# Optimization experiments

Measured on AMD Instinct MI355X. Metric: run time of the kernel, lower is better.

Reference implementation:

```python
import jax, jax.numpy as jnp
import numpy as np

N, E, B = 10000, 20000, 400
ND, ED, D = 32, 16, 64


def setup_inputs() -> dict:
    key = jax.random.key(0)
    ks = jax.random.split(key, 32)

    def lin(k, out_d, in_d):
        kw, kb = jax.random.split(k)
        s = 1.0 / np.sqrt(in_d)
        return (jax.random.uniform(kw, (out_d, in_d), jnp.float32, -s, s),
                jax.random.uniform(kb, (out_d,), jnp.float32, -s, s))

    W_in, b_in = lin(ks[0], D, ND)
    W_e1, b_e1 = lin(ks[1], D, ED)
    W_e2, b_e2 = lin(ks[2], D * D, D)
    b_conv = jax.random.uniform(ks[3], (D,), jnp.float32, -1/8.0, 1/8.0)
    W_ih, b_ih = lin(ks[4], 3 * D, D)
    W_hh, b_hh = lin(ks[5], 3 * D, D)
    W_ih_l, b_ih_l = lin(ks[6], 4 * D, 2 * D)
    W_hh_l, b_hh_l = lin(ks[7], 4 * D, D)
    W_o1, b_o1 = lin(ks[8], D, 2 * D)
    W_o2, b_o2 = lin(ks[9], 1, D)

    x = jax.random.normal(ks[10], (N, ND), jnp.float32)
    edge_attr = jax.random.normal(ks[11], (E, ED), jnp.float32)
    edge_index = jax.random.randint(ks[12], (2, E), 0, N, jnp.int64)
    batch = jnp.sort(jax.random.randint(ks[13], (N,), 0, B, jnp.int64))

    return dict(x=x, edge_attr=edge_attr,
                W_in=W_in, b_in=b_in, W_e1=W_e1, b_e1=b_e1, W_e2=W_e2, b_e2=b_e2,
                b_conv=b_conv, W_ih=W_ih, b_ih=b_ih, W_hh=W_hh, b_hh=b_hh,
                W_ih_l=W_ih_l, b_ih_l=b_ih_l, W_hh_l=W_hh_l, b_hh_l=b_hh_l,
                W_o1=W_o1, b_o1=b_o1, W_o2=W_o2, b_o2=b_o2,
                edge_index=edge_index, batch=batch)


def reference(x, edge_attr, W_in, b_in, W_e1, b_e1, W_e2, b_e2, b_conv,
              W_ih, b_ih, W_hh, b_hh, W_ih_l, b_ih_l, W_hh_l, b_hh_l,
              W_o1, b_o1, W_o2, b_o2, edge_index, batch):
    src, dst = edge_index[0], edge_index[1]

    # in_linear
    out = jax.nn.relu(x @ W_in.T + b_in)            # [N, D]
    h = out                                          # GRU hidden (layer=1, seq=1)

    # edge-conditioned weights: MLP(edge_attr) -> [E, D, D]
    ew = (jax.nn.relu(edge_attr @ W_e1.T + b_e1) @ W_e2.T + b_e2).reshape(E, D, D)
    cnt = jnp.maximum(jax.ops.segment_sum(jnp.ones((E,), x.dtype), dst, N), 1.0)

    for _ in range(3):
        # NNConv: gather src nodes, per-edge matmul, scatter-mean to dst, + bias
        msg = jnp.einsum('ed,edf->ef', out[src], ew)                 # [E, D]
        agg = jax.ops.segment_sum(msg, dst, N) / cnt[:, None] + b_conv
        m = jax.nn.relu(agg)
        # GRU cell (torch gate order r, z, n)
        gi = m @ W_ih.T + b_ih
        gh = h @ W_hh.T + b_hh
        i_r, i_z, i_n = jnp.split(gi, 3, axis=-1)
        h_r, h_z, h_n = jnp.split(gh, 3, axis=-1)
        r = jax.nn.sigmoid(i_r + h_r)
        z = jax.nn.sigmoid(i_z + h_z)
        n = jnp.tanh(i_n + r * h_n)
        h = (1.0 - z) * n + z * h
        out = h

    # Set2Set pooling, processing_steps=3
    q_star = jnp.zeros((B, 2 * D), x.dtype)
    hl = jnp.zeros((B, D), x.dtype)
    cl = jnp.zeros((B, D), x.dtype)
    for _ in range(3):
        g = q_star @ W_ih_l.T + b_ih_l + hl @ W_hh_l.T + b_hh_l
        gi_, gf_, gg_, go_ = jnp.split(g, 4, axis=-1)   # torch order i,f,g,o
        cl = jax.nn.sigmoid(gf_) * cl + jax.nn.sigmoid(gi_) * jnp.tanh(gg_)
        hl = jax.nn.sigmoid(go_) * jnp.tanh(cl)
        q = hl                                           # [B, D]
        e = jnp.sum(out * q[batch], axis=-1)             # [N]
        mmax = jax.ops.segment_max(e, batch, B)
        a = jnp.exp(e - mmax[batch])
        a = a / jax.ops.segment_sum(a, batch, B)[batch]
        r_ = jax.ops.segment_sum(a[:, None] * out, batch, B)  # [B, D]
        q_star = jnp.concatenate([q, r_], axis=-1)

    o = jax.nn.relu(q_star @ W_o1.T + b_o1) @ W_o2.T + b_o2
    return o.reshape(-1)
```

## Files before the change

### kernel.cpp

```cpp
#include <hip/hip_runtime.h>
#include <math.h>


#define Nn 10000
#define Ee 20000
#define Bb 400
#define KSTEPS 130
#define S2S_CHUNK 1024

typedef __attribute__((ext_vector_type(8))) short bf16x8_t;
typedef __attribute__((ext_vector_type(4))) float f32x4_t;

__device__ __forceinline__ float sigmoidf_(float x) { return 1.f / (1.f + expf(-x)); }

__device__ __forceinline__ void split8(const float* p, bf16x8_t& Ahi_, bf16x8_t& Alo_) {
    union { bf16x8_t v; unsigned u[4]; } hi, lo;
#pragma unroll
    for (int ii = 0; ii < 4; ++ii) {
        float pa = p[2 * ii], pb = p[2 * ii + 1];
        unsigned ua = __float_as_uint(pa), ub = __float_as_uint(pb);
        hi.u[ii] = (ua >> 16) | (ub & 0xFFFF0000u);
        float la = pa - __uint_as_float(ua & 0xFFFF0000u);
        float lb = pb - __uint_as_float(ub & 0xFFFF0000u);
        lo.u[ii] = (__float_as_uint(la) >> 16) | (__float_as_uint(lb) & 0xFFFF0000u);
    }
    Ahi_ = hi.v; Alo_ = lo.v;
}

__global__ __launch_bounds__(256) void k_in_linear(const float* __restrict__ x,
                                                   const float* __restrict__ Win,
                                                   const float* __restrict__ bin,
                                                   float* __restrict__ out) {
    int idx = blockIdx.x * 256 + threadIdx.x;
    if (idx >= Nn * 64) return;
    int n = idx >> 6, j = idx & 63;
    const float* xr = x + n * 32;
    const float* w = Win + j * 32;
    float acc = bin[j];
#pragma unroll
    for (int k = 0; k < 32; ++k) acc += xr[k] * w[k];
    out[idx] = fmaxf(acc, 0.f);
}

__global__ __launch_bounds__(256) void k_edge_mlp1(const float* __restrict__ ea,
                                                   const float* __restrict__ W1,
                                                   const float* __restrict__ b1,
                                                   float* __restrict__ eh) {
    int idx = blockIdx.x * 256 + threadIdx.x;
    if (idx >= Ee * 64) return;
    int e = idx >> 6, j = idx & 63;
    const float* ar = ea + e * 16;
    const float* w = W1 + j * 16;
    float acc = b1[j];
#pragma unroll
    for (int k = 0; k < 16; ++k) acc += ar[k] * w[k];
    eh[idx] = fmaxf(acc, 0.f);
}

__global__ __launch_bounds__(256) void k_make_Bfat(const float* __restrict__ W2,
                                                   const float* __restrict__ b2,
                                                   unsigned short* __restrict__ Bfat) {
    int idx = blockIdx.x * 256 + threadIdx.x;
    if (idx >= KSTEPS * 4096) return;
    int i  = idx & 7;
    int l  = (idx >> 3) & 63;
    int nq = (idx >> 9) & 3;
    int h  = (idx >> 11) & 1;
    int ks = idx >> 12;
    int kap = ks * 32 + (l >> 4) * 8 + i;
    int f = nq * 16 + (l & 15);
    float w;
    if (kap < 4096) {
        int q = kap >> 6, d = kap & 63;
        w = W2[(size_t)(d * 64 + f) * 64 + q];
    } else {
        int d = kap - 4096;
        w = b2[d * 64 + f];
    }
    unsigned u = __float_as_uint(w);
    unsigned short outv;
    if (h == 0) {
        outv = (unsigned short)(u >> 16);
    } else {
        float lo = w - __uint_as_float(u & 0xFFFF0000u);
        outv = (unsigned short)(__float_as_uint(lo) >> 16);
    }
    Bfat[idx] = outv;
}

__global__ __launch_bounds__(256) void k_make_Wg(const float* __restrict__ Wih,
                                                 const float* __restrict__ Whh,
                                                 unsigned short* __restrict__ Wg) {
    int idx = blockIdx.x * 256 + threadIdx.x;
    if (idx >= 4 * 2 * 16 * 64 * 8) return;
    int i  = idx & 7;
    int l  = (idx >> 3) & 63;
    int t  = (idx >> 9) & 15;
    int h  = (idx >> 13) & 1;
    int ks = idx >> 14;
    int k = ks * 32 + (l >> 4) * 8 + i;
    int u = t * 16 + (l & 15);
    int j = u & 63, part = u >> 6;
    float w = 0.f;
    if (part == 0) w = (k < 64) ? Wih[(size_t)j * 64 + k]          : Whh[(size_t)j * 64 + (k - 64)];
    if (part == 1) w = (k < 64) ? Wih[(size_t)(64 + j) * 64 + k]   : Whh[(size_t)(64 + j) * 64 + (k - 64)];
    if (part == 2) w = (k < 64) ? Wih[(size_t)(128 + j) * 64 + k]  : 0.f;
    if (part == 3) w = (k < 64) ? 0.f : Whh[(size_t)(128 + j) * 64 + (k - 64)];
    unsigned uu = __float_as_uint(w);
    unsigned short outv;
    if (h == 0) {
        outv = (unsigned short)(uu >> 16);
    } else {
        float lo = w - __uint_as_float(uu & 0xFFFF0000u);
        outv = (unsigned short)(__float_as_uint(lo) >> 16);
    }
    Wg[idx] = outv;
}

__global__ __launch_bounds__(256) void k_msg_mfma(const float* __restrict__ out,
                                                  const float* __restrict__ eh,
                                                  const unsigned short* __restrict__ Bfat,
                                                  const int* __restrict__ ei,
                                                  float* __restrict__ agg) {
    __shared__ float outs[64][68];
    __shared__ float ehs[64][68];
    __shared__ int dsts[64];
    int tid = threadIdx.x;
    int ebase = blockIdx.x * 64;
    int ksplit = blockIdx.y;

    {
        int el = tid >> 2, seg = tid & 3;
        int eg = ebase + el;
        bool v = eg < Ee;
        int s = 0, dn = 0;
        if (v) { s = ei[eg]; dn = ei[Ee + eg]; }
        if (seg == 0) dsts[el] = dn;
        const float* orow = out + (size_t)s * 64 + seg * 16;
        const float* erow = eh + (size_t)eg * 64 + seg * 16;
        float4 z = make_float4(0.f, 0.f, 0.f, 0.f);
#pragma unroll
        for (int c = 0; c < 4; ++c) {
            float4 ov = v ? *(const float4*)(orow + c * 4) : z;
            float4 ev = v ? *(const float4*)(erow + c * 4) : z;
            *(float4*)&outs[el][seg * 16 + c * 4] = ov;
            *(float4*)&ehs[el][seg * 16 + c * 4] = ev;
        }
    }
    __syncthreads();

    int lane = tid & 63;
    int wtile = tid >> 6;
    int m16 = lane & 15;
    int g = lane >> 4;
    int er = wtile * 16 + m16;

    f32x4_t acc[4];
#pragma unroll
    for (int nq = 0; nq < 4; ++nq) acc[nq] = (f32x4_t){0.f, 0.f, 0.f, 0.f};

    int ks0 = ksplit * 32 + (ksplit < 2 ? ksplit : 2);
    int ks1 = ks0 + (ksplit < 2 ? 33 : 32);

#pragma unroll 2
    for (int ks = ks0; ks < ks1; ++ks) {
        float ehq; int dbase;
        if (ks < 128) { ehq = ehs[er][ks >> 1]; dbase = (ks & 1) * 32 + g * 8; }
        else          { ehq = 1.f;              dbase = (ks - 128) * 32 + g * 8; }
        float4 o1 = *(const float4*)&outs[er][dbase];
        float4 o2 = *(const float4*)&outs[er][dbase + 4];
        float p[8] = {o1.x * ehq, o1.y * ehq, o1.z * ehq, o1.w * ehq,
                      o2.x * ehq, o2.y * ehq, o2.z * ehq, o2.w * ehq};
        bf16x8_t Ahi, Alo;
        split8(p, Ahi, Alo);
        const unsigned short* bstep = Bfat + (size_t)ks * 4096;
#pragma unroll
        for (int nq = 0; nq < 4; ++nq) {
            bf16x8_t bhi = *(const bf16x8_t*)(bstep + ((size_t)nq * 64 + lane) * 8);
            bf16x8_t blo = *(const bf16x8_t*)(bstep + ((size_t)(4 + nq) * 64 + lane) * 8);
            acc[nq] = __builtin_amdgcn_mfma_f32_16x16x32_bf16(Ahi, bhi, acc[nq], 0, 0, 0);
            acc[nq] = __builtin_amdgcn_mfma_f32_16x16x32_bf16(Ahi, blo, acc[nq], 0, 0, 0);
            acc[nq] = __builtin_amdgcn_mfma_f32_16x16x32_bf16(Alo, bhi, acc[nq], 0, 0, 0);
        }
    }

#pragma unroll
    for (int nq = 0; nq < 4; ++nq) {
#pragma unroll
        for (int r = 0; r < 4; ++r) {
            int el = wtile * 16 + g * 4 + r;
            int eg = ebase + el;
            if (eg < Ee)
                atomicAdd(&agg[(size_t)dsts[el] * 64 + nq * 16 + m16], acc[nq][r]);
        }
    }
}

__global__ __launch_bounds__(256) void k_gru_mfma(const float* __restrict__ agg,
                                                  const float* __restrict__ cnt,
                                                  const float* __restrict__ bconv,
                                                  const unsigned short* __restrict__ Wg,
                                                  const float* __restrict__ bih,
                                                  const float* __restrict__ bhh,
                                                  float* __restrict__ out) {
    __shared__ float ms[64][68];
    __shared__ float hs[64][68];
    int tid = threadIdx.x;
    int nbase = blockIdx.x * 64;

    {
        int nl = tid >> 2, seg = tid & 3;
        int ng = nbase + nl;
        bool v = ng < Nn;
        float c = v ? cnt[ng] : 1.f;
        c = c < 1.f ? 1.f : c;
        float rc = 1.f / c;
        const float* arow = agg + (size_t)ng * 64 + seg * 16;
        const float* hrow = out + (size_t)ng * 64 + seg * 16;
#pragma unroll
        for (int c4 = 0; c4 < 4; ++c4) {
            int col = seg * 16 + c4 * 4;
            float4 z = make_float4(0.f, 0.f, 0.f, 0.f);
            float4 av = v ? *(const float4*)(arow + c4 * 4) : z;
            float4 hv = v ? *(const float4*)(hrow + c4 * 4) : z;
            ms[nl][col + 0] = fmaxf(av.x * rc + bconv[col + 0], 0.f);
            ms[nl][col + 1] = fmaxf(av.y * rc + bconv[col + 1], 0.f);
            ms[nl][col + 2] = fmaxf(av.z * rc + bconv[col + 2], 0.f);
            ms[nl][col + 3] = fmaxf(av.w * rc + bconv[col + 3], 0.f);
            *(float4*)&hs[nl][col] = hv;
        }
    }
    __syncthreads();

    int lane = tid & 63;
    int wtile = tid >> 6;
    int m16 = lane & 15;
    int g = lane >> 4;
    int er = wtile * 16 + m16;

    f32x4_t acc[16];
#pragma unroll
    for (int t = 0; t < 16; ++t) acc[t] = (f32x4_t){0.f, 0.f, 0.f, 0.f};

#pragma unroll
    for (int ks = 0; ks < 4; ++ks) {
        const float* src = (ks < 2) ? &ms[er][ks * 32 + g * 8]
                                    : &hs[er][(ks - 2) * 32 + g * 8];
        float p[8];
#pragma unroll
        for (int ii = 0; ii < 8; ++ii) p[ii] = src[ii];
        bf16x8_t Ahi, Alo;
        split8(p, Ahi, Alo);
        const unsigned short* bstep = Wg + (size_t)ks * (2 * 16 * 512);
#pragma unroll
        for (int t = 0; t < 16; ++t) {
            bf16x8_t bhi = *(const bf16x8_t*)(bstep + ((size_t)t * 64 + lane) * 8);
            bf16x8_t blo = *(const bf16x8_t*)(bstep + ((size_t)(16 + t) * 64 + lane) * 8);
            acc[t] = __builtin_amdgcn_mfma_f32_16x16x32_bf16(Ahi, bhi, acc[t], 0, 0, 0);
            acc[t] = __builtin_amdgcn_mfma_f32_16x16x32_bf16(Ahi, blo, acc[t], 0, 0, 0);
            acc[t] = __builtin_amdgcn_mfma_f32_16x16x32_bf16(Alo, bhi, acc[t], 0, 0, 0);
        }
    }

#pragma unroll
    for (int t2 = 0; t2 < 4; ++t2) {
        int jj = t2 * 16 + m16;
        float br = bih[jj] + bhh[jj];
        float bz = bih[64 + jj] + bhh[64 + jj];
        float bin_ = bih[128 + jj];
        float bhn = bhh[128 + jj];
#pragma unroll
        for (int r = 0; r < 4; ++r) {
            int nl2 = wtile * 16 + g * 4 + r;
            int ng2 = nbase + nl2;
            if (ng2 >= Nn) continue;
            float rg = sigmoidf_(acc[t2][r] + br);
            float z  = sigmoidf_(acc[4 + t2][r] + bz);
            float nn = tanhf(acc[8 + t2][r] + bin_ + rg * (acc[12 + t2][r] + bhn));
            float hv = hs[nl2][jj];
            out[(size_t)ng2 * 64 + jj] = (1.f - z) * nn + z * hv;
        }
    }
}

__global__ __launch_bounds__(256) void k_count_deg(const int* __restrict__ ei,
                                                   float* __restrict__ cnt) {
    int e = blockIdx.x * 256 + threadIdx.x;
    if (e >= Ee) return;
    atomicAdd(&cnt[ei[Ee + e]], 1.f);
}

__global__ __launch_bounds__(256) void k_count_batch(const int* __restrict__ batch,
                                                     int* __restrict__ bcount) {
    int n = blockIdx.x * 256 + threadIdx.x;
    if (n >= Nn) return;
    atomicAdd(&bcount[batch[n]], 1);
}

__global__ __launch_bounds__(64) void k_scan_batch(const int* __restrict__ bcount,
                                                   int* __restrict__ bstart) {
    int lane = threadIdx.x;
    const int PER = (Bb + 63) / 64;
    int base = lane * PER;
    int v[PER];
    int s = 0;
#pragma unroll
    for (int i = 0; i < PER; ++i) {
        int idx = base + i;
        int c = (idx < Bb) ? bcount[idx] : 0;
        v[i] = s;
        s += c;
    }
    int inc = s;
#pragma unroll
    for (int o = 1; o < 64; o <<= 1) {
        int t = __shfl_up(inc, o, 64);
        if (lane >= o) inc += t;
    }
    int excl = inc - s;
    int total = __shfl(inc, 63, 64);
#pragma unroll
    for (int i = 0; i < PER; ++i) {
        int idx = base + i;
        if (idx < Bb) bstart[idx] = excl + v[i];
    }
    if (lane == 63) bstart[Bb] = total;
}

__device__ __forceinline__ float block_reduce_max_(float v, float* red, int tid) {
#pragma unroll
    for (int o = 32; o; o >>= 1) v = fmaxf(v, __shfl_xor(v, o, 64));
    if ((tid & 63) == 0) red[tid >> 6] = v;
    __syncthreads();
    float r = fmaxf(fmaxf(red[0], red[1]), fmaxf(red[2], red[3]));
    __syncthreads();
    return r;
}
__device__ __forceinline__ float block_reduce_sum_(float v, float* red, int tid) {
#pragma unroll
    for (int o = 32; o; o >>= 1) v += __shfl_xor(v, o, 64);
    if ((tid & 63) == 0) red[tid >> 6] = v;
    __syncthreads();
    float r = (red[0] + red[1]) + (red[2] + red[3]);
    __syncthreads();
    return r;
}

__global__ __launch_bounds__(256) void k_set2set(const float* __restrict__ out,
                                                 const int* __restrict__ bstart,
                                                 const float* __restrict__ Wil,
                                                 const float* __restrict__ bil,
                                                 const float* __restrict__ Whl,
                                                 const float* __restrict__ bhl,
                                                 const float* __restrict__ Wo1,
                                                 const float* __restrict__ bo1,
                                                 const float* __restrict__ Wo2,
                                                 const float* __restrict__ bo2,
                                                 float* __restrict__ outp) {
    __shared__ float qs[128];
    __shared__ float hs2[64];
    __shared__ float cs[64];
    __shared__ float g_lds[256];
    __shared__ float e_lds[S2S_CHUNK];
    __shared__ float red[4];
    __shared__ float rpart[4][64];

    int b = blockIdx.x, tid = threadIdx.x;
    int lane = tid & 63, wv = tid >> 6;
    int s = bstart[b], eend = bstart[b + 1];
    int cntb = eend - s;

    if (tid < 128) qs[tid] = 0.f;
    if (tid < 64) { hs2[tid] = 0.f; cs[tid] = 0.f; }
    __syncthreads();

    for (int step = 0; step < 3; ++step) {
        {
            int u = tid;
            float acc = bil[u] + bhl[u];
            const float4* wi = (const float4*)(Wil + (size_t)u * 128);
#pragma unroll
            for (int k4 = 0; k4 < 32; ++k4) {
                float4 w = wi[k4];
                acc += qs[k4 * 4 + 0] * w.x + qs[k4 * 4 + 1] * w.y +
                       qs[k4 * 4 + 2] * w.z + qs[k4 * 4 + 3] * w.w;
            }
            const float4* wh = (const float4*)(Whl + (size_t)u * 64);
#pragma unroll
            for (int k4 = 0; k4 < 16; ++k4) {
                float4 w = wh[k4];
                acc += hs2[k4 * 4 + 0] * w.x + hs2[k4 * 4 + 1] * w.y +
                       hs2[k4 * 4 + 2] * w.z + hs2[k4 * 4 + 3] * w.w;
            }
            g_lds[u] = acc;
        }
        __syncthreads();
        if (tid < 64) {
            float c = sigmoidf_(g_lds[64 + tid]) * cs[tid] +
                      sigmoidf_(g_lds[tid]) * tanhf(g_lds[128 + tid]);
            cs[tid] = c;
            float h = sigmoidf_(g_lds[192 + tid]) * tanhf(c);
            hs2[tid] = h;
            qs[tid] = h;
        }
        __syncthreads();

        float gmax = -INFINITY, gsum = 0.f, racc = 0.f;
        for (int c0 = s; c0 < eend; c0 += S2S_CHUNK) {
            int clen = min(S2S_CHUNK, eend - c0);
            for (int i = tid; i < clen; i += 256) {
                const float4* orow = (const float4*)(out + (size_t)(c0 + i) * 64);
                float a0 = 0.f, a1 = 0.f, a2 = 0.f, a3 = 0.f;
#pragma unroll
                for (int k4 = 0; k4 < 16; k4 += 4) {
                    float4 o0 = orow[k4], o1 = orow[k4 + 1], o2 = orow[k4 + 2], o3 = orow[k4 + 3];
                    a0 += o0.x * qs[k4 * 4 + 0]  + o0.y * qs[k4 * 4 + 1]  + o0.z * qs[k4 * 4 + 2]  + o0.w * qs[k4 * 4 + 3];
                    a1 += o1.x * qs[k4 * 4 + 4]  + o1.y * qs[k4 * 4 + 5]  + o1.z * qs[k4 * 4 + 6]  + o1.w * qs[k4 * 4 + 7];
                    a2 += o2.x * qs[k4 * 4 + 8]  + o2.y * qs[k4 * 4 + 9]  + o2.z * qs[k4 * 4 + 10] + o2.w * qs[k4 * 4 + 11];
                    a3 += o3.x * qs[k4 * 4 + 12] + o3.y * qs[k4 * 4 + 13] + o3.z * qs[k4 * 4 + 14] + o3.w * qs[k4 * 4 + 15];
                }
                e_lds[i] = (a0 + a1) + (a2 + a3);
            }
            __syncthreads();
            float m = -INFINITY;
            for (int i = tid; i < clen; i += 256) m = fmaxf(m, e_lds[i]);
            float cmax = block_reduce_max_(m, red, tid);
            float nm = fmaxf(gmax, cmax);
            float scale = expf(gmax - nm);
            gsum *= scale; racc *= scale;
            float lsum = 0.f;
            for (int i = tid; i < clen; i += 256) {
                float av = expf(e_lds[i] - nm);
                e_lds[i] = av;
                lsum += av;
            }
            gsum += block_reduce_sum_(lsum, red, tid);
            for (int i = wv; i < clen; i += 4)
                racc += e_lds[i] * out[(size_t)(c0 + i) * 64 + lane];
            gmax = nm;
            __syncthreads();
        }
        rpart[wv][lane] = racc;
        __syncthreads();
        if (tid < 64) {
            float r = (rpart[0][tid] + rpart[1][tid]) + (rpart[2][tid] + rpart[3][tid]);
            qs[64 + tid] = (cntb > 0) ? r / gsum : 0.f;
        }
        __syncthreads();
    }

    if (tid < 64) {
        float acc = bo1[tid];
        const float4* w = (const float4*)(Wo1 + (size_t)tid * 128);
#pragma unroll
        for (int k4 = 0; k4 < 32; ++k4) {
            float4 wv4 = w[k4];
            acc += qs[k4 * 4 + 0] * wv4.x + qs[k4 * 4 + 1] * wv4.y +
                   qs[k4 * 4 + 2] * wv4.z + qs[k4 * 4 + 3] * wv4.w;
        }
        acc = fmaxf(acc, 0.f);
        float t = acc * Wo2[tid];
#pragma unroll
        for (int o = 32; o; o >>= 1) t += __shfl_xor(t, o, 64);
        if (tid == 0) outp[b] = t + bo2[0];
    }
}

extern "C" void kernel_launch(void* const* d_in, const int* in_sizes, int n_in,
                              void* d_out, int out_size, void* d_ws, size_t ws_size,
                              hipStream_t stream) {
    const float* x        = (const float*)d_in[0];
    const float* ea       = (const float*)d_in[1];
    const float* W_in     = (const float*)d_in[2];
    const float* b_in     = (const float*)d_in[3];
    const float* W_e1     = (const float*)d_in[4];
    const float* b_e1     = (const float*)d_in[5];
    const float* W_e2     = (const float*)d_in[6];
    const float* b_e2     = (const float*)d_in[7];
    const float* b_conv   = (const float*)d_in[8];
    const float* W_ih     = (const float*)d_in[9];
    const float* b_ih     = (const float*)d_in[10];
    const float* W_hh     = (const float*)d_in[11];
    const float* b_hh     = (const float*)d_in[12];
    const float* W_ih_l   = (const float*)d_in[13];
    const float* b_ih_l   = (const float*)d_in[14];
    const float* W_hh_l   = (const float*)d_in[15];
    const float* b_hh_l   = (const float*)d_in[16];
    const float* W_o1     = (const float*)d_in[17];
    const float* b_o1     = (const float*)d_in[18];
    const float* W_o2     = (const float*)d_in[19];
    const float* b_o2     = (const float*)d_in[20];
    const int*   ei       = (const int*)d_in[21];
    const int*   batch    = (const int*)d_in[22];
    float* outp = (float*)d_out;

    char* base = (char*)d_ws;
    size_t off = 0;
    auto carve = [&](size_t bytes) -> void* {
        void* p = base + off;
        off = (off + bytes + 255) & ~(size_t)255;
        return p;
    };
    float* out    = (float*)carve((size_t)Nn * 64 * 4);
    float* agg    = (float*)carve((size_t)Nn * 64 * 4);
    float* eh     = (float*)carve((size_t)Ee * 64 * 4);
    unsigned short* Bfat = (unsigned short*)carve((size_t)KSTEPS * 4096 * 2);
    unsigned short* Wg   = (unsigned short*)carve((size_t)4 * 2 * 16 * 64 * 8 * 2);
    float* cnt    = (float*)carve((size_t)Nn * 4);
    int*   bcount = (int*)carve((size_t)Bb * 4);
    int*   bstart = (int*)carve((size_t)(Bb + 1) * 4);
    if (off > ws_size) return;

    hipMemsetAsync(cnt, 0, (size_t)Nn * 4, stream);
    hipMemsetAsync(bcount, 0, (size_t)Bb * 4, stream);

    k_in_linear<<<(Nn * 64) / 256, 256, 0, stream>>>(x, W_in, b_in, out);
    k_edge_mlp1<<<(Ee * 64) / 256, 256, 0, stream>>>(ea, W_e1, b_e1, eh);
    k_make_Bfat<<<(KSTEPS * 4096) / 256, 256, 0, stream>>>(W_e2, b_e2, Bfat);
    k_make_Wg<<<(4 * 2 * 16 * 64 * 8) / 256, 256, 0, stream>>>(W_ih, W_hh, Wg);
    k_count_deg<<<(Ee + 255) / 256, 256, 0, stream>>>(ei, cnt);
    k_count_batch<<<(Nn + 255) / 256, 256, 0, stream>>>(batch, bcount);
    k_scan_batch<<<1, 64, 0, stream>>>(bcount, bstart);

    int eblocks = (Ee + 63) / 64;
    int nblocks = (Nn + 63) / 64;
    for (int it = 0; it < 3; ++it) {
        hipMemsetAsync(agg, 0, (size_t)Nn * 64 * 4, stream);
        k_msg_mfma<<<dim3(eblocks, 4), 256, 0, stream>>>(out, eh, Bfat, ei, agg);
        k_gru_mfma<<<nblocks, 256, 0, stream>>>(agg, cnt, b_conv, Wg, b_ih, b_hh, out);
    }

    k_set2set<<<Bb, 256, 0, stream>>>(out, bstart, W_ih_l, b_ih_l, W_hh_l, b_hh_l,
                                      W_o1, b_o1, W_o2, b_o2, outp);
}
```

Measured before the change: 374.8 us.

## Shrink message-kernel LDS with swizzled tile and sliced edge weights

The message kernel now stages only the slice of edge-hidden values its K-split actually uses. It drops padding on the gathered node-feature tile in favour of an XOR swizzle to avoid bank conflicts, and reads destination indices directly in the epilogue instead of through shared memory. Launch bounds request 7 blocks per CU. The smaller LDS footprint is meant to raise occupancy and cut redundant global loads of edge-hidden data. The cost is some extra index arithmetic and a possible register-pressure squeeze from the occupancy hint.

```diff
diff --git a/kernel.cpp b/kernel.cpp
--- a/kernel.cpp
+++ b/kernel.cpp
@@ -117,35 +117,38 @@
     Wg[idx] = outv;
 }
 
-__global__ __launch_bounds__(256) void k_msg_mfma(const float* __restrict__ out,
-                                                  const float* __restrict__ eh,
-                                                  const unsigned short* __restrict__ Bfat,
-                                                  const int* __restrict__ ei,
-                                                  float* __restrict__ agg) {
-    __shared__ float outs[64][68];
-    __shared__ float ehs[64][68];
-    __shared__ int dsts[64];
+__global__ __launch_bounds__(256, 7) void k_msg_mfma(const float* __restrict__ out,
+                                                     const float* __restrict__ eh,
+                                                     const unsigned short* __restrict__ Bfat,
+                                                     const int* __restrict__ ei,
+                                                     float* __restrict__ agg) {
+    __shared__ float outs[64][64];
+    __shared__ float ehs[64][20];
     int tid = threadIdx.x;
     int ebase = blockIdx.x * 64;
     int ksplit = blockIdx.y;
+
+    int ks0 = ksplit * 32 + (ksplit < 2 ? ksplit : 2);
+    int ks1 = ks0 + (ksplit < 2 ? 33 : 32);
+    int q0 = ks0 >> 1;
+    int qn = ((min(ks1, 128) - 1) >> 1) - q0 + 1;
 
     {
         int el = tid >> 2, seg = tid & 3;
         int eg = ebase + el;
         bool v = eg < Ee;
-        int s = 0, dn = 0;
-        if (v) { s = ei[eg]; dn = ei[Ee + eg]; }
-        if (seg == 0) dsts[el] = dn;
+        int s = v ? ei[eg] : 0;
         const float* orow = out + (size_t)s * 64 + seg * 16;
-        const float* erow = eh + (size_t)eg * 64 + seg * 16;
         float4 z = make_float4(0.f, 0.f, 0.f, 0.f);
 #pragma unroll
         for (int c = 0; c < 4; ++c) {
             float4 ov = v ? *(const float4*)(orow + c * 4) : z;
-            float4 ev = v ? *(const float4*)(erow + c * 4) : z;
-            *(float4*)&outs[el][seg * 16 + c * 4] = ov;
-            *(float4*)&ehs[el][seg * 16 + c * 4] = ev;
-        }
+            int f = (seg * 4 + c) ^ (el & 7);
+            *(float4*)&outs[el][f * 4] = ov;
+        }
+        const float* erow = eh + (size_t)eg * 64;
+        for (int j = seg; j < qn; j += 4)
+            ehs[el][j] = v ? erow[q0 + j] : 0.f;
     }
     __syncthreads();
 
@@ -154,21 +157,18 @@
     int m16 = lane & 15;
     int g = lane >> 4;
     int er = wtile * 16 + m16;
+    int esw = er & 7;
 
     f32x4_t acc[4];
 #pragma unroll
     for (int nq = 0; nq < 4; ++nq) acc[nq] = (f32x4_t){0.f, 0.f, 0.f, 0.f};
-
-    int ks0 = ksplit * 32 + (ksplit < 2 ? ksplit : 2);
-    int ks1 = ks0 + (ksplit < 2 ? 33 : 32);
 
 #pragma unroll 2
     for (int ks = ks0; ks < ks1; ++ks) {
-        float ehq; int dbase;
-        if (ks < 128) { ehq = ehs[er][ks >> 1]; dbase = (ks & 1) * 32 + g * 8; }
-        else          { ehq = 1.f;              dbase = (ks - 128) * 32 + g * 8; }
-        float4 o1 = *(const float4*)&outs[er][dbase];
-        float4 o2 = *(const float4*)&outs[er][dbase + 4];
+        float ehq = (ks < 128) ? ehs[er][(ks >> 1) - q0] : 1.f;
+        int fbase = (ks & 1) * 8 + g * 2;
+        float4 o1 = *(const float4*)&outs[er][(fbase ^ esw) * 4];
+        float4 o2 = *(const float4*)&outs[er][((fbase + 1) ^ esw) * 4];
         float p[8] = {o1.x * ehq, o1.y * ehq, o1.z * ehq, o1.w * ehq,
                       o2.x * ehq, o2.y * ehq, o2.z * ehq, o2.w * ehq};
         bf16x8_t Ahi, Alo;
@@ -185,14 +185,14 @@
     }
 
 #pragma unroll
-    for (int nq = 0; nq < 4; ++nq) {
-#pragma unroll
-        for (int r = 0; r < 4; ++r) {
-            int el = wtile * 16 + g * 4 + r;
-            int eg = ebase + el;
-            if (eg < Ee)
-                atomicAdd(&agg[(size_t)dsts[el] * 64 + nq * 16 + m16], acc[nq][r]);
-        }
+    for (int r = 0; r < 4; ++r) {
+        int el = wtile * 16 + g * 4 + r;
+        int eg = ebase + el;
+        if (eg >= Ee) continue;
+        int dn = ei[Ee + eg];
+#pragma unroll
+        for (int nq = 0; nq < 4; ++nq)
+            atomicAdd(&agg[(size_t)dn * 64 + nq * 16 + m16], acc[nq][r]);
     }
 }
 
```

Result: slower. 386.2 us (+3.0%).
